# Kernel tuning notes

Hardware: AMD Instinct MI355X
Metric: run time of the kernel (lower is better)

## Reference

```python
import jax, jax.numpy as jnp
import numpy as np

N_HEADS = 16

def setup_inputs() -> dict:
    key = jax.random.key(0)
    ks = jax.random.split(key, 7)
    B, S, D = 2, 2048, 1024
    sc = 0.02
    return {
        "x": jax.random.normal(ks[0], (B, S, D), dtype=jnp.float32),
        "Wq": jax.random.normal(ks[1], (D, D), dtype=jnp.float32) * sc,
        "bq": jax.random.normal(ks[2], (D,), dtype=jnp.float32) * sc,
        "Wk": jax.random.normal(ks[3], (D, D), dtype=jnp.float32) * sc,
        "bk": jax.random.normal(ks[4], (D,), dtype=jnp.float32) * sc,
        "Wv": jax.random.normal(ks[5], (D, D), dtype=jnp.float32) * sc,
        "bv": jax.random.normal(ks[6], (D,), dtype=jnp.float32) * sc,
    }

def reference(x, Wq, bq, Wk, bk, Wv, bv):
    B, S, D = x.shape
    H = N_HEADS
    W = D // H  # head width
    # torch Linear: y = x @ W.T + b
    q = x @ Wq.T + bq
    k = x @ Wk.T + bk
    v = x @ Wv.T + bv
    # split last dim into (H, W) and move heads forward: (B, H, S, W)
    q = q.reshape(B, S, H, W).transpose(0, 2, 1, 3)
    k = k.reshape(B, S, H, W).transpose(0, 2, 1, 3)
    v = v.reshape(B, S, H, W).transpose(0, 2, 1, 3)
    scores = jnp.einsum("bhqw,bhkw->bhqk", q, k) / jnp.sqrt(jnp.asarray(W, x.dtype))
    # original applies softmax, (dropout=identity at eval), then softmax AGAIN
    scores = jax.nn.softmax(scores, axis=-1)
    scores = jax.nn.softmax(scores, axis=-1)
    h = jnp.einsum("bhqk,bhkw->bhqw", scores, v)
    h = h.transpose(0, 2, 1, 3).reshape(B, S, D)
    return h
```

## Files before the change

kernel.cpp:

```cpp
#include <hip/hip_runtime.h>
#include <cstdint>
#include <cstddef>

typedef __bf16 bf16_t;
typedef __bf16 bf16x4 __attribute__((ext_vector_type(4)));
typedef __bf16 bf16x8 __attribute__((ext_vector_type(8)));
typedef float f32x4 __attribute__((ext_vector_type(4)));

typedef __attribute__((address_space(1))) unsigned int gu32;
typedef __attribute__((address_space(3))) unsigned int lu32;

#define MFMA16(a, b, c) __builtin_amdgcn_mfma_f32_16x16x32_bf16((a), (b), (c), 0, 0, 0)

__device__ __forceinline__ void gload_lds16(const void* g, void* l) {
    __builtin_amdgcn_global_load_lds((gu32*)const_cast<void*>(g), (lu32*)l, 16, 0, 0);
}

__global__ __launch_bounds__(256) void cvt_bf16(
    const float* __restrict__ x, const float* __restrict__ Wq,
    const float* __restrict__ Wk, const float* __restrict__ Wv,
    bf16_t* __restrict__ xb, bf16_t* __restrict__ Wqb,
    bf16_t* __restrict__ Wkb, bf16_t* __restrict__ Wvb)
{
    const int z = blockIdx.z;
    const float* src = (z == 0) ? x : (z == 1) ? Wq : (z == 2) ? Wk : Wv;
    bf16_t* dst      = (z == 0) ? xb : (z == 1) ? Wqb : (z == 2) ? Wkb : Wvb;
    const int n = (z == 0) ? 4096 * 1024 : 1024 * 1024;
    const int stride = gridDim.x * blockDim.x * 4;
    for (int i = (blockIdx.x * blockDim.x + threadIdx.x) * 4; i < n; i += stride) {
        const float4 f = *(const float4*)(src + i);
        bf16x4 o; o[0] = (bf16_t)f.x; o[1] = (bf16_t)f.y; o[2] = (bf16_t)f.z; o[3] = (bf16_t)f.w;
        *(bf16x4*)(dst + i) = o;
    }
}

__global__ __launch_bounds__(512) void qkv_gemm_bf16(
    const bf16_t* __restrict__ xb,
    const bf16_t* __restrict__ W0b, const float* __restrict__ b0,
    const bf16_t* __restrict__ W1b, const float* __restrict__ b1,
    const bf16_t* __restrict__ W2b, const float* __restrict__ b2,
    bf16_t* __restrict__ Qo, bf16_t* __restrict__ Ko, bf16_t* __restrict__ VTo,
    float* __restrict__ Vp)
{
    const int z = blockIdx.z;
    const bf16_t* Wm = (z == 0) ? W0b : (z == 1) ? W1b : W2b;
    const float* bia = (z == 0) ? b0 : (z == 1) ? b1 : b2;

    __shared__ bf16_t As[2][128 * 32];
    __shared__ bf16_t Bs[2][128 * 32];

    const int tid  = threadIdx.x;
    const int lane = tid & 63;
    const int wv   = tid >> 6;
    const int quad = lane >> 4;
    const int l16  = lane & 15;
    const int wm   = wv >> 1;
    const int wn   = wv & 1;
    const int m0   = blockIdx.x * 128;
    const int n0   = blockIdx.y * 128;

    const int rs = tid >> 2;
    const int gs = ((tid & 3) ^ ((rs >> 1) & 3)) * 8;
    const int fp = (quad ^ ((l16 >> 1) & 3)) * 8;

    f32x4 acc[2][4];
    for (int i = 0; i < 2; i++)
        for (int j = 0; j < 4; j++) acc[i][j] = (f32x4)0.0f;

    gload_lds16(xb + (size_t)(m0 + rs) * 1024 + gs, &As[0][(wv * 64) * 8]);
    gload_lds16(Wm + (size_t)(n0 + rs) * 1024 + gs, &Bs[0][(wv * 64) * 8]);

#pragma unroll 2
    for (int kt = 0; kt < 32; kt++) {
        const int cur = kt & 1, nxt = cur ^ 1;
        __syncthreads();
        if (kt < 31) {
            const int kp = (kt + 1) * 32;
            gload_lds16(xb + (size_t)(m0 + rs) * 1024 + kp + gs, &As[nxt][(wv * 64) * 8]);
            gload_lds16(Wm + (size_t)(n0 + rs) * 1024 + kp + gs, &Bs[nxt][(wv * 64) * 8]);
        }
        bf16x8 af[2], bfr[4];
        for (int mt = 0; mt < 2; mt++)
            af[mt] = *(const bf16x8*)&As[cur][(wm * 32 + mt * 16 + l16) * 32 + fp];
        for (int nt = 0; nt < 4; nt++)
            bfr[nt] = *(const bf16x8*)&Bs[cur][(wn * 64 + nt * 16 + l16) * 32 + fp];
        for (int mt = 0; mt < 2; mt++)
            for (int nt = 0; nt < 4; nt++)
                acc[mt][nt] = MFMA16(af[mt], bfr[nt], acc[mt][nt]);
    }

    float bv[4];
    for (int nt = 0; nt < 4; nt++)
        bv[nt] = bia[n0 + wn * 64 + nt * 16 + l16];

    if (z < 2) {
        bf16_t* out = (z == 0) ? Qo : Ko;
        for (int mt = 0; mt < 2; mt++) {
            const int mrow = m0 + wm * 32 + mt * 16 + quad * 4;
            for (int nt = 0; nt < 4; nt++) {
                const int n = n0 + wn * 64 + nt * 16 + l16;
                for (int r = 0; r < 4; r++)
                    out[(size_t)(mrow + r) * 1024 + n] = (bf16_t)(acc[mt][nt][r] + bv[nt]);
            }
        }
    } else {
        const int h = blockIdx.y * 2 + wn;
        float psum[4] = {0.f, 0.f, 0.f, 0.f};
        for (int mt = 0; mt < 2; mt++) {
            const int sg = m0 + wm * 32 + mt * 16 + quad * 4;
            const int bb = sg >> 11;
            const int s  = sg & 2047;
            for (int nt = 0; nt < 4; nt++) {
                const int w = nt * 16 + l16;
                bf16x4 pk;
                for (int r = 0; r < 4; r++) {
                    pk[r] = (bf16_t)(acc[mt][nt][r] + bv[nt]);
                    psum[nt] += (float)pk[r];
                }
                *(bf16x4*)(VTo + ((size_t)((bb * 16 + h) * 64 + w)) * 2048 + s) = pk;
            }
        }
        for (int nt = 0; nt < 4; nt++) {
            psum[nt] += __shfl_xor(psum[nt], 16, 64);
            psum[nt] += __shfl_xor(psum[nt], 32, 64);
        }
        float* red = (float*)&As[0][0];
        if (quad == 0)
            for (int nt = 0; nt < 4; nt++)
                red[(wv * 4 + nt) * 16 + l16] = psum[nt];
        __syncthreads();
        if (wm == 0 && quad == 0) {
            const int bb = m0 >> 11;
            const int j  = blockIdx.x & 15;
            for (int nt = 0; nt < 4; nt++) {
                float s4 = ((red[((wn + 0) * 4 + nt) * 16 + l16]
                           + red[((wn + 2) * 4 + nt) * 16 + l16])
                           + red[((wn + 4) * 4 + nt) * 16 + l16])
                           + red[((wn + 6) * 4 + nt) * 16 + l16];
                Vp[((size_t)((bb * 16 + h) * 64 + nt * 16 + l16)) * 16 + j] = s4;
            }
        }
    }
}

__global__ __launch_bounds__(512, 4) void attn(
    const bf16_t* __restrict__ Qg, const bf16_t* __restrict__ Kg,
    const bf16_t* __restrict__ VTg, const float* __restrict__ Vp,
    float* __restrict__ out)
{
    const int qt = blockIdx.x;
    const int h  = blockIdx.y;
    const int b  = blockIdx.z;

    const int tid  = threadIdx.x;
    const int wv   = tid >> 6;
    const int lane = tid & 63;
    const int quad = lane >> 4;
    const int l16  = lane & 15;

    const size_t base  = ((size_t)b * 2048) * 1024 + (size_t)h * 64;
    const size_t vbase = ((size_t)(b * 16 + h) * 64) * 2048;
    const int q0 = qt * 128;

    __shared__ bf16_t Ps[2][128 * 64];
    __shared__ bf16_t Ks[2][64 * 64];
    __shared__ bf16_t Vs[2][64 * 64];

    {
        const int c0 = tid, c1 = 512 + tid;
        const int r0 = c0 >> 3, g0 = ((c0 & 7) ^ (r0 & 7)) * 8;
        const int r1 = c1 >> 3, g1 = ((c1 & 7) ^ (r1 & 7)) * 8;
        gload_lds16(Qg + base + (size_t)(q0 + r0) * 1024 + g0, &Ps[0][(wv * 64) * 8]);
        gload_lds16(Qg + base + (size_t)(q0 + r1) * 1024 + g1, &Ps[0][(512 + wv * 64) * 8]);
    }
    const int rk = tid >> 3;
    const int gk = ((tid & 7) ^ (rk & 7)) * 8;
    gload_lds16(Kg + base + (size_t)rk * 1024 + gk, &Ks[0][(wv * 64) * 8]);
    gload_lds16(VTg + vbase + (size_t)rk * 2048 + gk, &Vs[0][(wv * 64) * 8]);

    const int fs0 = ((0 ^ quad) ^ (l16 & 7)) * 8;
    const int fs1 = ((4 ^ quad) ^ (l16 & 7)) * 8;
    const int rowA = (wv * 16 + l16) * 64;
    const int qrow = wv * 16 + l16;

    f32x4 oa[4], l1acc;
    for (int nt = 0; nt < 4; nt++) oa[nt] = (f32x4)0.0f;
    l1acc = (f32x4)0.0f;

    bf16x8 ones;
    for (int j = 0; j < 8; j++) ones[j] = (bf16_t)1.0f;

    __syncthreads();
    const bf16x8 aq0 = *(const bf16x8*)&Ps[0][rowA + fs0];
    const bf16x8 aq1 = *(const bf16x8*)&Ps[0][rowA + fs1];

    bf16x8 bv0[4], bv1[4];

    {
        gload_lds16(Kg + base + (size_t)(64 + rk) * 1024 + gk, &Ks[1][(wv * 64) * 8]);
        gload_lds16(VTg + vbase + (size_t)rk * 2048 + 64 + gk, &Vs[1][(wv * 64) * 8]);

        f32x4 sa[4];
        for (int nt = 0; nt < 4; nt++) sa[nt] = (f32x4)0.0f;
        for (int nt = 0; nt < 4; nt++) {
            bf16x8 kb = *(const bf16x8*)&Ks[0][(nt * 16 + l16) * 64 + fs0];
            sa[nt] = MFMA16(kb, aq0, sa[nt]);
        }
        for (int nt = 0; nt < 4; nt++) {
            bf16x8 kb = *(const bf16x8*)&Ks[0][(nt * 16 + l16) * 64 + fs1];
            sa[nt] = MFMA16(kb, aq1, sa[nt]);
        }
        for (int nt = 0; nt < 4; nt++) {
            bf16x4 pk;
            for (int r = 0; r < 4; r++)
                pk[r] = (bf16_t)__expf(sa[nt][r] * 0.125f);
            const int c = nt * 2 + (quad >> 1);
            *(bf16x4*)&Ps[0][qrow * 64 + ((c ^ (qrow & 7)) * 8) + (quad & 1) * 4] = pk;
        }
        for (int nt = 0; nt < 4; nt++)
            bv0[nt] = *(const bf16x8*)&Vs[0][(nt * 16 + l16) * 64 + fs0];
        for (int nt = 0; nt < 4; nt++)
            bv1[nt] = *(const bf16x8*)&Vs[0][(nt * 16 + l16) * 64 + fs1];
    }

#pragma unroll 2
    for (int kt = 1; kt < 32; kt++) {
        const int cur = kt & 1, prv = cur ^ 1;
        __syncthreads();

        const bf16x8 af0 = *(const bf16x8*)&Ps[prv][rowA + fs0];
        const bf16x8 af1 = *(const bf16x8*)&Ps[prv][rowA + fs1];

        if (kt < 31) {
            gload_lds16(Kg + base + (size_t)((kt + 1) * 64 + rk) * 1024 + gk,
                        &Ks[prv][(wv * 64) * 8]);
            gload_lds16(VTg + vbase + (size_t)rk * 2048 + (kt + 1) * 64 + gk,
                        &Vs[prv][(wv * 64) * 8]);
        }

        f32x4 sa[4];
        for (int nt = 0; nt < 4; nt++) sa[nt] = (f32x4)0.0f;
        for (int nt = 0; nt < 4; nt++) {
            bf16x8 kb = *(const bf16x8*)&Ks[cur][(nt * 16 + l16) * 64 + fs0];
            sa[nt] = MFMA16(kb, aq0, sa[nt]);
        }
        for (int nt = 0; nt < 4; nt++) {
            bf16x8 kb = *(const bf16x8*)&Ks[cur][(nt * 16 + l16) * 64 + fs1];
            sa[nt] = MFMA16(kb, aq1, sa[nt]);
        }

        l1acc = MFMA16(af0, ones, l1acc);
        for (int nt = 0; nt < 4; nt++) oa[nt] = MFMA16(af0, bv0[nt], oa[nt]);
        l1acc = MFMA16(af1, ones, l1acc);
        for (int nt = 0; nt < 4; nt++) oa[nt] = MFMA16(af1, bv1[nt], oa[nt]);

        for (int nt = 0; nt < 4; nt++)
            bv0[nt] = *(const bf16x8*)&Vs[cur][(nt * 16 + l16) * 64 + fs0];
        for (int nt = 0; nt < 4; nt++)
            bv1[nt] = *(const bf16x8*)&Vs[cur][(nt * 16 + l16) * 64 + fs1];

        for (int nt = 0; nt < 4; nt++) {
            bf16x4 pk;
            for (int r = 0; r < 4; r++)
                pk[r] = (bf16_t)__expf(sa[nt][r] * 0.125f);
            const int c = nt * 2 + (quad >> 1);
            *(bf16x4*)&Ps[cur][qrow * 64 + ((c ^ (qrow & 7)) * 8) + (quad & 1) * 4] = pk;
        }
    }

    {
        const bf16x8 af0 = *(const bf16x8*)&Ps[1][rowA + fs0];
        const bf16x8 af1 = *(const bf16x8*)&Ps[1][rowA + fs1];
        l1acc = MFMA16(af0, ones, l1acc);
        for (int nt = 0; nt < 4; nt++) oa[nt] = MFMA16(af0, bv0[nt], oa[nt]);
        l1acc = MFMA16(af1, ones, l1acc);
        for (int nt = 0; nt < 4; nt++) oa[nt] = MFMA16(af1, bv1[nt], oa[nt]);
    }

    float invq[4];
    for (int r = 0; r < 4; r++) invq[r] = 1.0f / l1acc[r];

    float vs[4];
    {
        const size_t vprow = (size_t)(b * 16 + h) * 64;
        for (int nt = 0; nt < 4; nt++) {
            const f32x4 p4 = *(const f32x4*)&Vp[(vprow + nt * 16 + l16) * 16 + quad * 4];
            float t = (p4[0] + p4[1]) + (p4[2] + p4[3]);
            t += __shfl_xor(t, 16, 64);
            t += __shfl_xor(t, 32, 64);
            vs[nt] = t;
        }
    }

    const float inv_denom = 1.0f / 2049.0f;
    for (int nt = 0; nt < 4; nt++) {
        for (int r = 0; r < 4; r++) {
            const int srow = q0 + wv * 16 + quad * 4 + r;
            out[((size_t)b * 2048 + srow) * 1024 + (size_t)h * 64 + nt * 16 + l16] =
                (vs[nt] + oa[nt][r] * invq[r]) * inv_denom;
        }
    }
}

extern "C" void kernel_launch(void* const* d_in, const int* in_sizes, int n_in,
                              void* d_out, int out_size, void* d_ws, size_t ws_size,
                              hipStream_t stream) {
    const float* x  = (const float*)d_in[0];
    const float* Wq = (const float*)d_in[1];
    const float* bq = (const float*)d_in[2];
    const float* Wk = (const float*)d_in[3];
    const float* bk = (const float*)d_in[4];
    const float* Wv = (const float*)d_in[5];
    const float* bv = (const float*)d_in[6];

    bf16_t* Qw  = (bf16_t*)d_ws;
    bf16_t* Kw  = Qw + (size_t)4096 * 1024;
    bf16_t* VTw = Kw + (size_t)4096 * 1024;
    float*  Vp  = (float*)(VTw + (size_t)4096 * 1024);

    bf16_t* xb  = (bf16_t*)d_out;
    bf16_t* Wqb = xb + (size_t)4096 * 1024;
    bf16_t* Wkb = Wqb + (size_t)1024 * 1024;
    bf16_t* Wvb = Wkb + (size_t)1024 * 1024;

    cvt_bf16<<<dim3(1024, 1, 4), 256, 0, stream>>>(x, Wq, Wk, Wv, xb, Wqb, Wkb, Wvb);
    qkv_gemm_bf16<<<dim3(32, 8, 3), 512, 0, stream>>>(
        xb, Wqb, bq, Wkb, bk, Wvb, bv, Qw, Kw, VTw, Vp);
    attn<<<dim3(16, 16, 2), 512, 0, stream>>>(Qw, Kw, VTw, Vp, (float*)d_out);
}
```

Baseline: 166.7 us.

## Re-partition attention waves into 32-query groups with split-K PV and LDS reduction

Each wave now owns 32 query rows and half of each 64-key tile instead of 16 query rows and all keys. This lets each K fragment and each V fragment loaded from LDS feed two MFMAs. The PV partial sums of the two half-waves are combined through LDS at the end with extra barriers. The 1/sqrt(d) scale is folded into Q in the projection epilogue, which removes a multiply per exp. In exchange the kernel holds more accumulator registers and adds an epilogue reduction, which may cut occupancy.

```diff
diff --git a/kernel.cpp b/kernel.cpp
--- a/kernel.cpp
+++ b/kernel.cpp
@@ -95,12 +95,13 @@
 
     if (z < 2) {
         bf16_t* out = (z == 0) ? Qo : Ko;
+        const float scl = (z == 0) ? 0.125f : 1.0f;
         for (int mt = 0; mt < 2; mt++) {
             const int mrow = m0 + wm * 32 + mt * 16 + quad * 4;
             for (int nt = 0; nt < 4; nt++) {
                 const int n = n0 + wn * 64 + nt * 16 + l16;
                 for (int r = 0; r < 4; r++)
-                    out[(size_t)(mrow + r) * 1024 + n] = (bf16_t)(acc[mt][nt][r] + bv[nt]);
+                    out[(size_t)(mrow + r) * 1024 + n] = (bf16_t)((acc[mt][nt][r] + bv[nt]) * scl);
             }
         }
     } else {
@@ -157,6 +158,8 @@
     const int lane = tid & 63;
     const int quad = lane >> 4;
     const int l16  = lane & 15;
+    const int qg   = wv >> 1;
+    const int sh   = wv & 1;
 
     const size_t base  = ((size_t)b * 2048) * 1024 + (size_t)h * 64;
     const size_t vbase = ((size_t)(b * 16 + h) * 64) * 2048;
@@ -180,47 +183,57 @@
 
     const int fs0 = ((0 ^ quad) ^ (l16 & 7)) * 8;
     const int fs1 = ((4 ^ quad) ^ (l16 & 7)) * 8;
-    const int rowA = (wv * 16 + l16) * 64;
-    const int qrow = wv * 16 + l16;
-
-    f32x4 oa[4], l1acc;
-    for (int nt = 0; nt < 4; nt++) oa[nt] = (f32x4)0.0f;
-    l1acc = (f32x4)0.0f;
+    const int fsA = sh ? fs1 : fs0;
+
+    const int qr0 = qg * 32 + l16;
+    const int qr1 = qg * 32 + 16 + l16;
+
+    f32x4 oa[2][4], l1acc[2];
+    for (int qs = 0; qs < 2; qs++) {
+        for (int nt = 0; nt < 4; nt++) oa[qs][nt] = (f32x4)0.0f;
+        l1acc[qs] = (f32x4)0.0f;
+    }
 
     bf16x8 ones;
     for (int j = 0; j < 8; j++) ones[j] = (bf16_t)1.0f;
 
     __syncthreads();
-    const bf16x8 aq0 = *(const bf16x8*)&Ps[0][rowA + fs0];
-    const bf16x8 aq1 = *(const bf16x8*)&Ps[0][rowA + fs1];
-
-    bf16x8 bv0[4], bv1[4];
+
+    bf16x8 aq[2][2];
+    aq[0][0] = *(const bf16x8*)&Ps[0][qr0 * 64 + fs0];
+    aq[0][1] = *(const bf16x8*)&Ps[0][qr0 * 64 + fs1];
+    aq[1][0] = *(const bf16x8*)&Ps[0][qr1 * 64 + fs0];
+    aq[1][1] = *(const bf16x8*)&Ps[0][qr1 * 64 + fs1];
+
+    bf16x8 bvf[4];
 
     {
         gload_lds16(Kg + base + (size_t)(64 + rk) * 1024 + gk, &Ks[1][(wv * 64) * 8]);
         gload_lds16(VTg + vbase + (size_t)rk * 2048 + 64 + gk, &Vs[1][(wv * 64) * 8]);
 
-        f32x4 sa[4];
-        for (int nt = 0; nt < 4; nt++) sa[nt] = (f32x4)0.0f;
-        for (int nt = 0; nt < 4; nt++) {
-            bf16x8 kb = *(const bf16x8*)&Ks[0][(nt * 16 + l16) * 64 + fs0];
-            sa[nt] = MFMA16(kb, aq0, sa[nt]);
-        }
-        for (int nt = 0; nt < 4; nt++) {
-            bf16x8 kb = *(const bf16x8*)&Ks[0][(nt * 16 + l16) * 64 + fs1];
-            sa[nt] = MFMA16(kb, aq1, sa[nt]);
-        }
-        for (int nt = 0; nt < 4; nt++) {
-            bf16x4 pk;
-            for (int r = 0; r < 4; r++)
-                pk[r] = (bf16_t)__expf(sa[nt][r] * 0.125f);
-            const int c = nt * 2 + (quad >> 1);
-            *(bf16x4*)&Ps[0][qrow * 64 + ((c ^ (qrow & 7)) * 8) + (quad & 1) * 4] = pk;
-        }
+        f32x4 sa[2][2];
+        for (int st = 0; st < 2; st++)
+            for (int qs = 0; qs < 2; qs++) sa[st][qs] = (f32x4)0.0f;
+        for (int st = 0; st < 2; st++) {
+            const int srow = (sh * 32 + st * 16 + l16) * 64;
+            bf16x8 kb0 = *(const bf16x8*)&Ks[0][srow + fs0];
+            bf16x8 kb1 = *(const bf16x8*)&Ks[0][srow + fs1];
+            for (int qs = 0; qs < 2; qs++) {
+                sa[st][qs] = MFMA16(kb0, aq[qs][0], sa[st][qs]);
+                sa[st][qs] = MFMA16(kb1, aq[qs][1], sa[st][qs]);
+            }
+        }
+        for (int st = 0; st < 2; st++)
+            for (int qs = 0; qs < 2; qs++) {
+                bf16x4 pk;
+                for (int r = 0; r < 4; r++)
+                    pk[r] = (bf16_t)__expf(sa[st][qs][r]);
+                const int qrow = qg * 32 + qs * 16 + l16;
+                const int cc   = sh * 4 + st * 2 + (quad >> 1);
+                *(bf16x4*)&Ps[0][qrow * 64 + ((cc ^ (qrow & 7)) * 8) + (quad & 1) * 4] = pk;
+            }
         for (int nt = 0; nt < 4; nt++)
-            bv0[nt] = *(const bf16x8*)&Vs[0][(nt * 16 + l16) * 64 + fs0];
-        for (int nt = 0; nt < 4; nt++)
-            bv1[nt] = *(const bf16x8*)&Vs[0][(nt * 16 + l16) * 64 + fs1];
+            bvf[nt] = *(const bf16x8*)&Vs[0][(nt * 16 + l16) * 64 + fsA];
     }
 
 #pragma unroll 2
@@ -228,8 +241,8 @@
         const int cur = kt & 1, prv = cur ^ 1;
         __syncthreads();
 
-        const bf16x8 af0 = *(const bf16x8*)&Ps[prv][rowA + fs0];
-        const bf16x8 af1 = *(const bf16x8*)&Ps[prv][rowA + fs1];
+        const bf16x8 af0 = *(const bf16x8*)&Ps[prv][qr0 * 64 + fsA];
+        const bf16x8 af1 = *(const bf16x8*)&Ps[prv][qr1 * 64 + fsA];
 
         if (kt < 31) {
             gload_lds16(Kg + base + (size_t)((kt + 1) * 64 + rk) * 1024 + gk,
@@ -238,50 +251,76 @@
                         &Vs[prv][(wv * 64) * 8]);
         }
 
-        f32x4 sa[4];
-        for (int nt = 0; nt < 4; nt++) sa[nt] = (f32x4)0.0f;
+        f32x4 sa[2][2];
+        for (int st = 0; st < 2; st++)
+            for (int qs = 0; qs < 2; qs++) sa[st][qs] = (f32x4)0.0f;
+        for (int st = 0; st < 2; st++) {
+            const int srow = (sh * 32 + st * 16 + l16) * 64;
+            bf16x8 kb0 = *(const bf16x8*)&Ks[cur][srow + fs0];
+            bf16x8 kb1 = *(const bf16x8*)&Ks[cur][srow + fs1];
+            for (int qs = 0; qs < 2; qs++) {
+                sa[st][qs] = MFMA16(kb0, aq[qs][0], sa[st][qs]);
+                sa[st][qs] = MFMA16(kb1, aq[qs][1], sa[st][qs]);
+            }
+        }
+
+        l1acc[0] = MFMA16(af0, ones, l1acc[0]);
+        l1acc[1] = MFMA16(af1, ones, l1acc[1]);
         for (int nt = 0; nt < 4; nt++) {
-            bf16x8 kb = *(const bf16x8*)&Ks[cur][(nt * 16 + l16) * 64 + fs0];
-            sa[nt] = MFMA16(kb, aq0, sa[nt]);
-        }
+            oa[0][nt] = MFMA16(af0, bvf[nt], oa[0][nt]);
+            oa[1][nt] = MFMA16(af1, bvf[nt], oa[1][nt]);
+        }
+
+        for (int nt = 0; nt < 4; nt++)
+            bvf[nt] = *(const bf16x8*)&Vs[cur][(nt * 16 + l16) * 64 + fsA];
+
+        for (int st = 0; st < 2; st++)
+            for (int qs = 0; qs < 2; qs++) {
+                bf16x4 pk;
+                for (int r = 0; r < 4; r++)
+                    pk[r] = (bf16_t)__expf(sa[st][qs][r]);
+                const int qrow = qg * 32 + qs * 16 + l16;
+                const int cc   = sh * 4 + st * 2 + (quad >> 1);
+                *(bf16x4*)&Ps[cur][qrow * 64 + ((cc ^ (qrow & 7)) * 8) + (quad & 1) * 4] = pk;
+            }
+    }
+
+    {
+        const bf16x8 af0 = *(const bf16x8*)&Ps[1][qr0 * 64 + fsA];
+        const bf16x8 af1 = *(const bf16x8*)&Ps[1][qr1 * 64 + fsA];
+        l1acc[0] = MFMA16(af0, ones, l1acc[0]);
+        l1acc[1] = MFMA16(af1, ones, l1acc[1]);
         for (int nt = 0; nt < 4; nt++) {
-            bf16x8 kb = *(const bf16x8*)&Ks[cur][(nt * 16 + l16) * 64 + fs1];
-            sa[nt] = MFMA16(kb, aq1, sa[nt]);
-        }
-
-        l1acc = MFMA16(af0, ones, l1acc);
-        for (int nt = 0; nt < 4; nt++) oa[nt] = MFMA16(af0, bv0[nt], oa[nt]);
-        l1acc = MFMA16(af1, ones, l1acc);
-        for (int nt = 0; nt < 4; nt++) oa[nt] = MFMA16(af1, bv1[nt], oa[nt]);
-
-        for (int nt = 0; nt < 4; nt++)
-            bv0[nt] = *(const bf16x8*)&Vs[cur][(nt * 16 + l16) * 64 + fs0];
-        for (int nt = 0; nt < 4; nt++)
-            bv1[nt] = *(const bf16x8*)&Vs[cur][(nt * 16 + l16) * 64 + fs1];
-
-        for (int nt = 0; nt < 4; nt++) {
-            bf16x4 pk;
-            for (int r = 0; r < 4; r++)
-                pk[r] = (bf16_t)__expf(sa[nt][r] * 0.125f);
-            const int c = nt * 2 + (quad >> 1);
-            *(bf16x4*)&Ps[cur][qrow * 64 + ((c ^ (qrow & 7)) * 8) + (quad & 1) * 4] = pk;
-        }
-    }
-
-    {
-        const bf16x8 af0 = *(const bf16x8*)&Ps[1][rowA + fs0];
-        const bf16x8 af1 = *(const bf16x8*)&Ps[1][rowA + fs1];
-        l1acc = MFMA16(af0, ones, l1acc);
-        for (int nt = 0; nt < 4; nt++) oa[nt] = MFMA16(af0, bv0[nt], oa[nt]);
-        l1acc = MFMA16(af1, ones, l1acc);
-        for (int nt = 0; nt < 4; nt++) oa[nt] = MFMA16(af1, bv1[nt], oa[nt]);
-    }
-
-    float invq[4];
-    for (int r = 0; r < 4; r++) invq[r] = 1.0f / l1acc[r];
-
-    float vs[4];
-    {
+            oa[0][nt] = MFMA16(af0, bvf[nt], oa[0][nt]);
+            oa[1][nt] = MFMA16(af1, bvf[nt], oa[1][nt]);
+        }
+    }
+
+    __syncthreads();
+    f32x4* P4 = (f32x4*)&Ps[0][0];
+    f32x4* L4 = (f32x4*)&Ks[0][0];
+    if (sh == 1) {
+        const int bi = (qg * 64 + lane) * 8;
+        for (int qs = 0; qs < 2; qs++)
+            for (int nt = 0; nt < 4; nt++)
+                P4[bi + qs * 4 + nt] = oa[qs][nt];
+        L4[(qg * 64 + lane) * 2 + 0] = l1acc[0];
+        L4[(qg * 64 + lane) * 2 + 1] = l1acc[1];
+    }
+    __syncthreads();
+    if (sh == 0) {
+        const int bi = (qg * 64 + lane) * 8;
+        for (int qs = 0; qs < 2; qs++)
+            for (int nt = 0; nt < 4; nt++)
+                oa[qs][nt] += P4[bi + qs * 4 + nt];
+        l1acc[0] += L4[(qg * 64 + lane) * 2 + 0];
+        l1acc[1] += L4[(qg * 64 + lane) * 2 + 1];
+
+        float invq[2][4];
+        for (int qs = 0; qs < 2; qs++)
+            for (int r = 0; r < 4; r++) invq[qs][r] = 1.0f / l1acc[qs][r];
+
+        float vs[4];
         const size_t vprow = (size_t)(b * 16 + h) * 64;
         for (int nt = 0; nt < 4; nt++) {
             const f32x4 p4 = *(const f32x4*)&Vp[(vprow + nt * 16 + l16) * 16 + quad * 4];
@@ -290,15 +329,15 @@
             t += __shfl_xor(t, 32, 64);
             vs[nt] = t;
         }
-    }
-
-    const float inv_denom = 1.0f / 2049.0f;
-    for (int nt = 0; nt < 4; nt++) {
-        for (int r = 0; r < 4; r++) {
-            const int srow = q0 + wv * 16 + quad * 4 + r;
-            out[((size_t)b * 2048 + srow) * 1024 + (size_t)h * 64 + nt * 16 + l16] =
-                (vs[nt] + oa[nt][r] * invq[r]) * inv_denom;
-        }
+
+        const float inv_denom = 1.0f / 2049.0f;
+        for (int qs = 0; qs < 2; qs++)
+            for (int nt = 0; nt < 4; nt++)
+                for (int r = 0; r < 4; r++) {
+                    const int srow = q0 + qg * 32 + qs * 16 + quad * 4 + r;
+                    out[((size_t)b * 2048 + srow) * 1024 + (size_t)h * 64 + nt * 16 + l16] =
+                        (vs[nt] + oa[qs][nt][r] * invq[qs][r]) * inv_denom;
+                }
     }
 }
 
```

Result: no change. 165.1 us (-1.0%).
